# Kernel tuning notes

Hardware: AMD Instinct MI355X
Metric: run time of the kernel (lower is better)

## Reference

```python
import jax, jax.numpy as jnp
import numpy as np

N_KERNELS = 5
MUL_FACTOR = 2.0


def setup_inputs() -> dict:
    key = jax.random.key(0)
    X = jax.random.normal(key, (4096, 64), dtype=jnp.float32)
    # bandwidth multipliers: mul_factor ** (arange(K) - K//2)
    bandwidth_multipliers = (MUL_FACTOR ** (jnp.arange(N_KERNELS) - N_KERNELS // 2)).astype(jnp.float32)
    return {"X": X, "bandwidth_multipliers": bandwidth_multipliers}


def reference(X, bandwidth_multipliers):
    # squared pairwise euclidean distances: ||x_i||^2 + ||x_j||^2 - 2 x_i . x_j
    sq_norms = jnp.sum(X * X, axis=-1)                      # [N]
    gram = X @ X.T                                          # [N, N]
    L2 = jnp.maximum(sq_norms[:, None] + sq_norms[None, :] - 2.0 * gram, 0.0)  # [N, N]

    # bandwidth estimate uses .data in torch -> stop_gradient
    n = X.shape[0]
    bw = jax.lax.stop_gradient(L2.sum()) / (n * n - n)

    # sum over K bandwidth-scaled RBF kernels
    scales = bw * bandwidth_multipliers                     # [K]
    out = jnp.sum(jnp.exp(-L2[None, :, :] / scales[:, None, None]), axis=0)  # [N, N]
    return out
```

## Files before the change

### kernel.cpp

```cpp
#include <hip/hip_runtime.h>
#include <hip/hip_bf16.h>
#include <math.h>

#define N 4096
#define PB 32

typedef __attribute__((ext_vector_type(8))) short short8;
typedef __attribute__((ext_vector_type(4))) float floatx4;

__device__ float g_ws[PB * 66];

__device__ inline unsigned bfpk(float a, float b) {
    unsigned ua = __float_as_uint(a), ub = __float_as_uint(b);
    ua = (ua + 0x7fffu + ((ua >> 16) & 1u)) >> 16;
    ub = (ub + 0x7fffu + ((ub >> 16) & 1u)) >> 16;
    return ua | (ub << 16);
}

__device__ inline uint4 pack8(float4 f0, float4 f1) {
    uint4 r;
    r.x = bfpk(f0.x, f0.y);
    r.y = bfpk(f0.z, f0.w);
    r.z = bfpk(f1.x, f1.y);
    r.w = bfpk(f1.z, f1.w);
    return r;
}

__global__ __launch_bounds__(256) void prep_kernel(const float* __restrict__ X) {
    __shared__ float sm[256];
    __shared__ float ssum[4];
    const int lane = threadIdx.x & 63, w = threadIdx.x >> 6;
    const int b = blockIdx.x;
    const int row0 = b * 128 + w * 32;
    float mloc = 0.f, Sloc = 0.f;
    #pragma unroll
    for (int rr = 0; rr < 32; ++rr) {
        float x = X[(size_t)(row0 + rr) * 64 + lane];
        mloc += x; Sloc += x * x;
    }
    sm[threadIdx.x] = mloc;
    #pragma unroll
    for (int off = 1; off < 64; off <<= 1) Sloc += __shfl_xor(Sloc, off, 64);
    if (lane == 0) ssum[w] = Sloc;
    __syncthreads();
    if (threadIdx.x < 64) {
        g_ws[b * 66 + threadIdx.x] =
            sm[threadIdx.x] + sm[64 + threadIdx.x] + sm[128 + threadIdx.x] + sm[192 + threadIdx.x];
    } else if (threadIdx.x == 64) {
        g_ws[b * 66 + 64] = ssum[0] + ssum[1] + ssum[2] + ssum[3];
    }
}

__global__ __launch_bounds__(256) void rbf_kernel(const float* __restrict__ X,
                                                  float* __restrict__ out) {
    __shared__ uint4 lA[512];
    __shared__ uint4 lB[1024];
    __shared__ float sR[64];
    __shared__ float sC[128];

    const int t_ = threadIdx.x;
    const int b  = blockIdx.x;

    int I, J, h;
    if (b < 64) {
        I = J = b >> 1; h = b & 1;
    } else {
        int t = (b - 64) >> 1; h = (b - 64) & 1;
        int i = (int)((63.0f - sqrtf((float)(3969 - 8 * t))) * 0.5f);
        while (31 * (i + 1) - ((i + 1) * i) / 2 <= t) ++i;
        while (31 * i - (i * (i - 1)) / 2 > t) --i;
        int oi = 31 * i - (i * (i - 1)) / 2;
        I = i; J = i + 1 + (t - oi);
    }
    const int rowBase = I * 128 + h * 64;
    const int colBase = J * 128;
    const bool offdiag = (I != J);

    #pragma unroll
    for (int i = 0; i < 4; ++i) {
        int slot = i * 256 + t_;
        int r = slot >> 3, g = slot & 7;
        int c = g ^ (r & 7);
        const float4* p = (const float4*)(X + (size_t)(colBase + r) * 64 + c * 8);
        float4 f0 = p[0], f1 = p[1];
        lB[slot] = pack8(f0, f1);
        float nb = f0.x*f0.x + f0.y*f0.y + f0.z*f0.z + f0.w*f0.w
                 + f1.x*f1.x + f1.y*f1.y + f1.z*f1.z + f1.w*f1.w;
        #pragma unroll
        for (int off = 1; off < 8; off <<= 1) nb += __shfl_xor(nb, off, 64);
        if (g == 0) sC[r] = nb;
    }
    #pragma unroll
    for (int i = 0; i < 2; ++i) {
        int slot = i * 256 + t_;
        int r = slot >> 3, g = slot & 7;
        int c = g ^ (r & 7);
        const float4* p = (const float4*)(X + (size_t)(rowBase + r) * 64 + c * 8);
        float4 f0 = p[0], f1 = p[1];
        lA[slot] = pack8(f0, f1);
        float na = f0.x*f0.x + f0.y*f0.y + f0.z*f0.z + f0.w*f0.w
                 + f1.x*f1.x + f1.y*f1.y + f1.z*f1.z + f1.w*f1.w;
        #pragma unroll
        for (int off = 1; off < 8; off <<= 1) na += __shfl_xor(na, off, 64);
        if (g == 0) sR[r] = na;
    }

    const int lane = t_ & 63;
    float mv = 0.f;
    #pragma unroll 8
    for (int pb = 0; pb < PB; ++pb) mv += g_ws[pb * 66 + lane];
    float Sv = (lane < PB) ? g_ws[lane * 66 + 64] : 0.f;
    float mm = mv * mv;
    #pragma unroll
    for (int off = 1; off < 64; off <<= 1) {
        mm += __shfl_xor(mm, off, 64);
        Sv += __shfl_xor(Sv, off, 64);
    }
    float sumL2 = 2.0f * (float)N * Sv - 2.0f * mm;
    const float c1q = -1.4426950408889634f * 0.25f * (float)((size_t)N * N - N) / sumL2;

    __syncthreads();

    const int wave = t_ >> 6;
    const int lr = lane & 15, q = lane >> 4;

    int r1 = wave * 16 + lr;
    short8 a0 = *reinterpret_cast<const short8*>(&lA[8 * r1 + ((q    ) ^ (r1 & 7))]);
    short8 a1 = *reinterpret_cast<const short8*>(&lA[8 * r1 + ((q + 4) ^ (r1 & 7))]);

    floatx4 acc[8];
    #pragma unroll
    for (int tj = 0; tj < 8; ++tj) acc[tj] = (floatx4){0.f, 0.f, 0.f, 0.f};

    #pragma unroll
    for (int tj = 0; tj < 8; ++tj) {
        int r2 = tj * 16 + lr;
        short8 b0 = *reinterpret_cast<const short8*>(&lB[8 * r2 + ((q    ) ^ (r2 & 7))]);
        short8 b1 = *reinterpret_cast<const short8*>(&lB[8 * r2 + ((q + 4) ^ (r2 & 7))]);
        acc[tj] = __builtin_amdgcn_mfma_f32_16x16x32_bf16(a0, b0, acc[tj], 0, 0, 0);
        acc[tj] = __builtin_amdgcn_mfma_f32_16x16x32_bf16(a1, b1, acc[tj], 0, 0, 0);
    }

    const int rb = wave * 16 + q * 4;
    float sr0 = sR[rb], sr1 = sR[rb + 1], sr2 = sR[rb + 2], sr3 = sR[rb + 3];
    #pragma unroll
    for (int tj = 0; tj < 8; ++tj) {
        int cl = tj * 16 + lr;
        float scj = sC[cl];
        size_t col = (size_t)(colBase + cl);
        float4 tp;
        #pragma unroll
        for (int p = 0; p < 4; ++p) {
            float srp = (p == 0) ? sr0 : (p == 1) ? sr1 : (p == 2) ? sr2 : sr3;
            float d2 = srp + scj - 2.0f * acc[tj][p];
            d2 = fmaxf(d2, 0.0f);
            float u  = __builtin_amdgcn_exp2f(d2 * c1q);
            float s1 = u * u;
            float e  = s1 * s1;
            float e2 = e * e;
            float e4 = e2 * e2;
            float val = e4 + e2 + e + s1 + u;
            out[(size_t)(rowBase + rb + p) * N + col] = val;
            ((float*)&tp)[p] = val;
        }
        if (offdiag) {
            *reinterpret_cast<float4*>(&out[col * (size_t)N + (rowBase + rb)]) = tp;
        }
    }
}

extern "C" void kernel_launch(void* const* d_in, const int* in_sizes, int n_in,
                              void* d_out, int out_size, void* d_ws, size_t ws_size,
                              hipStream_t stream) {
    const float* X = (const float*)d_in[0];
    float* out = (float*)d_out;
    (void)d_ws; (void)ws_size;

    prep_kernel<<<PB, 256, 0, stream>>>(X);
    rbf_kernel<<<1056, 256, 0, stream>>>(X, out);
}
```

Before: 86.16 us.

## Precompute bf16-packed X and row norms in prep kernel; use nontemporal stores

```diff
diff --git a/kernel.cpp b/kernel.cpp
--- a/kernel.cpp
+++ b/kernel.cpp
@@ -9,6 +9,8 @@
 typedef __attribute__((ext_vector_type(4))) float floatx4;
 
 __device__ float g_ws[PB * 66];
+__device__ float g_nrm[N];
+__device__ uint4 g_X[N * 8];
 
 __device__ inline unsigned bfpk(float a, float b) {
     unsigned ua = __float_as_uint(a), ub = __float_as_uint(b);
@@ -31,6 +33,7 @@
     __shared__ float ssum[4];
     const int lane = threadIdx.x & 63, w = threadIdx.x >> 6;
     const int b = blockIdx.x;
+
     const int row0 = b * 128 + w * 32;
     float mloc = 0.f, Sloc = 0.f;
     #pragma unroll
@@ -49,14 +52,31 @@
     } else if (threadIdx.x == 64) {
         g_ws[b * 66 + 64] = ssum[0] + ssum[1] + ssum[2] + ssum[3];
     }
+
+    const int r = b * 128 + (threadIdx.x >> 1);
+    const int h = threadIdx.x & 1;
+    const float4* pr = (const float4*)(X + (size_t)r * 64 + h * 32);
+    float4 f0 = pr[0], f1 = pr[1], f2 = pr[2], f3 = pr[3];
+    float4 f4 = pr[4], f5 = pr[5], f6 = pr[6], f7 = pr[7];
+    float nh = f0.x*f0.x + f0.y*f0.y + f0.z*f0.z + f0.w*f0.w
+             + f1.x*f1.x + f1.y*f1.y + f1.z*f1.z + f1.w*f1.w
+             + f2.x*f2.x + f2.y*f2.y + f2.z*f2.z + f2.w*f2.w
+             + f3.x*f3.x + f3.y*f3.y + f3.z*f3.z + f3.w*f3.w
+             + f4.x*f4.x + f4.y*f4.y + f4.z*f4.z + f4.w*f4.w
+             + f5.x*f5.x + f5.y*f5.y + f5.z*f5.z + f5.w*f5.w
+             + f6.x*f6.x + f6.y*f6.y + f6.z*f6.z + f6.w*f6.w
+             + f7.x*f7.x + f7.y*f7.y + f7.z*f7.z + f7.w*f7.w;
+    nh += __shfl_xor(nh, 1, 64);
+    if (h == 0) g_nrm[r] = nh;
+    const int sw = r & 7;
+    g_X[r * 8 + ((4*h + 0) ^ sw)] = pack8(f0, f1);
+    g_X[r * 8 + ((4*h + 1) ^ sw)] = pack8(f2, f3);
+    g_X[r * 8 + ((4*h + 2) ^ sw)] = pack8(f4, f5);
+    g_X[r * 8 + ((4*h + 3) ^ sw)] = pack8(f6, f7);
 }
 
-__global__ __launch_bounds__(256) void rbf_kernel(const float* __restrict__ X,
-                                                  float* __restrict__ out) {
-    __shared__ uint4 lA[512];
+__global__ __launch_bounds__(256) void rbf_kernel(float* __restrict__ out) {
     __shared__ uint4 lB[1024];
-    __shared__ float sR[64];
-    __shared__ float sC[128];
 
     const int t_ = threadIdx.x;
     const int b  = blockIdx.x;
@@ -77,35 +97,25 @@
     const bool offdiag = (I != J);
 
     #pragma unroll
-    for (int i = 0; i < 4; ++i) {
-        int slot = i * 256 + t_;
-        int r = slot >> 3, g = slot & 7;
-        int c = g ^ (r & 7);
-        const float4* p = (const float4*)(X + (size_t)(colBase + r) * 64 + c * 8);
-        float4 f0 = p[0], f1 = p[1];
-        lB[slot] = pack8(f0, f1);
-        float nb = f0.x*f0.x + f0.y*f0.y + f0.z*f0.z + f0.w*f0.w
-                 + f1.x*f1.x + f1.y*f1.y + f1.z*f1.z + f1.w*f1.w;
-        #pragma unroll
-        for (int off = 1; off < 8; off <<= 1) nb += __shfl_xor(nb, off, 64);
-        if (g == 0) sC[r] = nb;
-    }
-    #pragma unroll
-    for (int i = 0; i < 2; ++i) {
-        int slot = i * 256 + t_;
-        int r = slot >> 3, g = slot & 7;
-        int c = g ^ (r & 7);
-        const float4* p = (const float4*)(X + (size_t)(rowBase + r) * 64 + c * 8);
-        float4 f0 = p[0], f1 = p[1];
-        lA[slot] = pack8(f0, f1);
-        float na = f0.x*f0.x + f0.y*f0.y + f0.z*f0.z + f0.w*f0.w
-                 + f1.x*f1.x + f1.y*f1.y + f1.z*f1.z + f1.w*f1.w;
-        #pragma unroll
-        for (int off = 1; off < 8; off <<= 1) na += __shfl_xor(na, off, 64);
-        if (g == 0) sR[r] = na;
-    }
+    for (int i = 0; i < 4; ++i)
+        lB[i * 256 + t_] = g_X[J * 1024 + i * 256 + t_];
 
     const int lane = t_ & 63;
+    const int wave = t_ >> 6;
+    const int lr = lane & 15, q = lane >> 4;
+
+    const int r1g = rowBase + wave * 16 + lr;
+    short8 a0 = *reinterpret_cast<const short8*>(&g_X[r1g * 8 + ((q    ) ^ (r1g & 7))]);
+    short8 a1 = *reinterpret_cast<const short8*>(&g_X[r1g * 8 + ((q + 4) ^ (r1g & 7))]);
+
+    const int rb = wave * 16 + q * 4;
+    float sr0 = g_nrm[rowBase + rb], sr1 = g_nrm[rowBase + rb + 1];
+    float sr2 = g_nrm[rowBase + rb + 2], sr3 = g_nrm[rowBase + rb + 3];
+    float sc0 = g_nrm[colBase + lr],       sc1 = g_nrm[colBase + 16 + lr];
+    float sc2 = g_nrm[colBase + 32 + lr],  sc3 = g_nrm[colBase + 48 + lr];
+    float sc4 = g_nrm[colBase + 64 + lr],  sc5 = g_nrm[colBase + 80 + lr];
+    float sc6 = g_nrm[colBase + 96 + lr],  sc7 = g_nrm[colBase + 112 + lr];
+
     float mv = 0.f;
     #pragma unroll 8
     for (int pb = 0; pb < PB; ++pb) mv += g_ws[pb * 66 + lane];
@@ -121,13 +131,6 @@
 
     __syncthreads();
 
-    const int wave = t_ >> 6;
-    const int lr = lane & 15, q = lane >> 4;
-
-    int r1 = wave * 16 + lr;
-    short8 a0 = *reinterpret_cast<const short8*>(&lA[8 * r1 + ((q    ) ^ (r1 & 7))]);
-    short8 a1 = *reinterpret_cast<const short8*>(&lA[8 * r1 + ((q + 4) ^ (r1 & 7))]);
-
     floatx4 acc[8];
     #pragma unroll
     for (int tj = 0; tj < 8; ++tj) acc[tj] = (floatx4){0.f, 0.f, 0.f, 0.f};
@@ -141,31 +144,42 @@
         acc[tj] = __builtin_amdgcn_mfma_f32_16x16x32_bf16(a1, b1, acc[tj], 0, 0, 0);
     }
 
-    const int rb = wave * 16 + q * 4;
-    float sr0 = sR[rb], sr1 = sR[rb + 1], sr2 = sR[rb + 2], sr3 = sR[rb + 3];
+    float* po0 = out + (size_t)(rowBase + rb + 0) * N + colBase + lr;
+    float* po1 = po0 + N;
+    float* po2 = po1 + N;
+    float* po3 = po2 + N;
+    float* pt  = out + (size_t)(colBase + lr) * N + rowBase + rb;
+
     #pragma unroll
     for (int tj = 0; tj < 8; ++tj) {
-        int cl = tj * 16 + lr;
-        float scj = sC[cl];
-        size_t col = (size_t)(colBase + cl);
-        float4 tp;
-        #pragma unroll
-        for (int p = 0; p < 4; ++p) {
-            float srp = (p == 0) ? sr0 : (p == 1) ? sr1 : (p == 2) ? sr2 : sr3;
-            float d2 = srp + scj - 2.0f * acc[tj][p];
-            d2 = fmaxf(d2, 0.0f);
-            float u  = __builtin_amdgcn_exp2f(d2 * c1q);
-            float s1 = u * u;
-            float e  = s1 * s1;
-            float e2 = e * e;
-            float e4 = e2 * e2;
-            float val = e4 + e2 + e + s1 + u;
-            out[(size_t)(rowBase + rb + p) * N + col] = val;
-            ((float*)&tp)[p] = val;
+        float scj = (tj == 0) ? sc0 : (tj == 1) ? sc1 : (tj == 2) ? sc2 : (tj == 3) ? sc3
+                  : (tj == 4) ? sc4 : (tj == 5) ? sc5 : (tj == 6) ? sc6 : sc7;
+        float b0 = sr0 + scj, b1 = sr1 + scj, b2 = sr2 + scj, b3 = sr3 + scj;
+        float d0 = fmaxf(fmaf(-2.0f, acc[tj][0], b0), 0.0f) * c1q;
+        float d1 = fmaxf(fmaf(-2.0f, acc[tj][1], b1), 0.0f) * c1q;
+        float d2 = fmaxf(fmaf(-2.0f, acc[tj][2], b2), 0.0f) * c1q;
+        float d3 = fmaxf(fmaf(-2.0f, acc[tj][3], b3), 0.0f) * c1q;
+        float u0 = __builtin_amdgcn_exp2f(d0);
+        float u1 = __builtin_amdgcn_exp2f(d1);
+        float u2 = __builtin_amdgcn_exp2f(d2);
+        float u3 = __builtin_amdgcn_exp2f(d3);
+        float s0 = u0*u0, e0 = s0*s0, e20 = e0*e0, e40 = e20*e20;
+        float s1 = u1*u1, e1 = s1*s1, e21 = e1*e1, e41 = e21*e21;
+        float s2 = u2*u2, e2 = s2*s2, e22 = e2*e2, e42 = e22*e22;
+        float s3 = u3*u3, e3 = s3*s3, e23 = e3*e3, e43 = e23*e23;
+        float v0 = e40 + e20 + e0 + s0 + u0;
+        float v1 = e41 + e21 + e1 + s1 + u1;
+        float v2 = e42 + e22 + e2 + s2 + u2;
+        float v3 = e43 + e23 + e3 + s3 + u3;
+        __builtin_nontemporal_store(v0, po0 + tj * 16);
+        __builtin_nontemporal_store(v1, po1 + tj * 16);
+        __builtin_nontemporal_store(v2, po2 + tj * 16);
+        __builtin_nontemporal_store(v3, po3 + tj * 16);
+        if (offdiag) {
+            floatx4 tv = {v0, v1, v2, v3};
+            __builtin_nontemporal_store(tv, reinterpret_cast<floatx4*>(pt));
         }
-        if (offdiag) {
-            *reinterpret_cast<float4*>(&out[col * (size_t)N + (rowBase + rb)]) = tp;
-        }
+        pt += (size_t)16 * N;
     }
 }
 
@@ -177,5 +191,5 @@
     (void)d_ws; (void)ws_size;
 
     prep_kernel<<<PB, 256, 0, stream>>>(X);
-    rbf_kernel<<<1056, 256, 0, stream>>>(X, out);
+    rbf_kernel<<<1056, 256, 0, stream>>>(out);
 }
```

Result: slower. 93.67 us (+8.7%).
